# Performance work log

Measured on AMD Instinct MI355X. Metric: run time of the kernel, lower is better.

The kernel has to match this reference:

```python
import jax, jax.numpy as jnp
import numpy as np

D_MODEL = 1024
H = 16
D_K = D_MODEL // H
D_FF = 4096
EPS = 1e-6


def layer_norm(x, alpha, bias):
    mean = jnp.mean(x, axis=-1, keepdims=True)
    var = jnp.mean((x - mean) ** 2, axis=-1, keepdims=True)  # unbiased=False
    return alpha * (x - mean) / jnp.sqrt(var + EPS) + bias


def setup_inputs() -> dict:
    key = jax.random.key(0)
    ks = jax.random.split(key, 8)
    B, S = 4, 2048
    sd = 1.0 / np.sqrt(D_MODEL)
    x = jax.random.normal(ks[0], (B, S, D_MODEL), dtype=jnp.float32)
    src_mask = jnp.ones((B, 1, S), dtype=jnp.int32)
    wq = jax.random.normal(ks[1], (D_MODEL, D_MODEL), jnp.float32) * sd
    wk = jax.random.normal(ks[2], (D_MODEL, D_MODEL), jnp.float32) * sd
    wv = jax.random.normal(ks[3], (D_MODEL, D_MODEL), jnp.float32) * sd
    wo = jax.random.normal(ks[4], (D_MODEL, D_MODEL), jnp.float32) * sd
    w1 = jax.random.normal(ks[5], (D_FF, D_MODEL), jnp.float32) * sd
    b1 = jnp.zeros((D_FF,), jnp.float32)
    w2 = jax.random.normal(ks[6], (D_MODEL, D_FF), jnp.float32) * (1.0 / np.sqrt(D_FF))
    b2 = jnp.zeros((D_MODEL,), jnp.float32)
    ln1_a = jnp.ones((D_MODEL,), jnp.float32)
    ln1_b = jnp.zeros((D_MODEL,), jnp.float32)
    ln2_a = jnp.ones((D_MODEL,), jnp.float32)
    ln2_b = jnp.zeros((D_MODEL,), jnp.float32)
    return dict(x=x, src_mask=src_mask, wq=wq, wk=wk, wv=wv, wo=wo,
                ln1_a=ln1_a, ln1_b=ln1_b, ln2_a=ln2_a, ln2_b=ln2_b,
                w1=w1, b1=b1, w2=w2, b2=b2)


def attention(xn, wq, wk, wv, wo, src_mask):
    B, S, _ = xn.shape
    # torch nn.Linear: y = x @ W.T
    q = (xn @ wq.T).reshape(B, S, H, D_K).transpose(0, 2, 1, 3)  # [B,H,S,Dk]
    k = (xn @ wk.T).reshape(B, S, H, D_K).transpose(0, 2, 1, 3)
    v = (xn @ wv.T).reshape(B, S, H, D_K).transpose(0, 2, 1, 3)
    scores = jnp.einsum('bhqd,bhkd->bhqk', q, k) / np.sqrt(D_K)
    m = src_mask[:, None, :, :]  # [B,1,1,S] from [B,1,S]
    scores = jnp.where(m == 0, -jnp.inf, scores)
    attn = jax.nn.softmax(scores, axis=-1)
    out = jnp.einsum('bhqk,bhkd->bhqd', attn, v)
    out = out.transpose(0, 2, 1, 3).reshape(B, S, D_MODEL)
    return out @ wo.T


def reference(x, src_mask, wq, wk, wv, wo, ln1_a, ln1_b, ln2_a, ln2_b, w1, b1, w2, b2):
    # pre-LN residual 1: self-attention
    xn = layer_norm(x, ln1_a, ln1_b)
    x = x + attention(xn, wq, wk, wv, wo, src_mask)
    # pre-LN residual 2: FFN
    xn = layer_norm(x, ln2_a, ln2_b)
    h = jax.nn.relu(xn @ w1.T + b1)
    x = x + (h @ w2.T + b2)
    return x
```

## Files before the change

kernel.cpp:

```cpp
#include <hip/hip_runtime.h>
#include <stdint.h>

typedef unsigned short u16;
typedef __bf16 bf16x8 __attribute__((ext_vector_type(8)));
typedef float   f32x4 __attribute__((ext_vector_type(4)));
typedef u16     u16x8 __attribute__((ext_vector_type(8)));
typedef u16     u16x4 __attribute__((ext_vector_type(4)));

__device__ __forceinline__ u16 f2bf(float f) {
    union { float f; uint32_t i; } c; c.f = f;
    uint32_t r = c.i + 0x7FFFu + ((c.i >> 16) & 1u);
    return (u16)(r >> 16);
}
__device__ __forceinline__ uint32_t cvt_pk_bf16(float lo, float hi) {
    uint32_t r;
    asm("v_cvt_pk_bf16_f32 %0, %1, %2" : "=v"(r) : "v"(lo), "v"(hi));
    return r;
}
__device__ __forceinline__ void gload_lds16(const u16* g, u16* l) {
    __builtin_amdgcn_global_load_lds(
        (__attribute__((address_space(1))) void*)(g),
        (__attribute__((address_space(3))) void*)(l), 16, 0, 0);
}

__global__ __launch_bounds__(256) void cvt_all(
    const float* __restrict__ wq, const float* __restrict__ wk,
    const float* __restrict__ wv, const float* __restrict__ wo,
    const float* __restrict__ w1, const float* __restrict__ w2,
    u16* __restrict__ wqb, u16* __restrict__ wkb, u16* __restrict__ wvb,
    u16* __restrict__ wob, u16* __restrict__ w1b, u16* __restrict__ w2b)
{
    int blk = blockIdx.x;
    const float* src; u16* dst; int off;
    if      (blk < 1024)  { src = wq; dst = wqb; off = blk; }
    else if (blk < 2048)  { src = wk; dst = wkb; off = blk - 1024; }
    else if (blk < 3072)  { src = wv; dst = wvb; off = blk - 2048; }
    else if (blk < 4096)  { src = wo; dst = wob; off = blk - 3072; }
    else if (blk < 8192)  { src = w1; dst = w1b; off = blk - 4096; }
    else                  { src = w2; dst = w2b; off = blk - 8192; }
    int i = off * 1024 + threadIdx.x * 4;
    float4 v = *(const float4*)(src + i);
    u16x4 o; o[0] = f2bf(v.x); o[1] = f2bf(v.y); o[2] = f2bf(v.z); o[3] = f2bf(v.w);
    *(u16x4*)(dst + i) = o;
}

__global__ __launch_bounds__(256) void ln_kernel(
    const float* __restrict__ x, const float* __restrict__ ga,
    const float* __restrict__ be, u16* __restrict__ out)
{
    const int D = 1024;
    int row  = blockIdx.x * 4 + (threadIdx.x >> 6);
    int lane = threadIdx.x & 63;
    const float* xr = x + (size_t)row * D + lane * 16;
    float f[16];
#pragma unroll
    for (int i = 0; i < 4; ++i) *(float4*)&f[i * 4] = *(const float4*)(xr + i * 4);
    float s = 0.f, s2 = 0.f;
#pragma unroll
    for (int i = 0; i < 16; ++i) { s += f[i]; s2 += f[i] * f[i]; }
#pragma unroll
    for (int off = 1; off < 64; off <<= 1) {
        s  += __shfl_xor(s,  off, 64);
        s2 += __shfl_xor(s2, off, 64);
    }
    float mean = s * (1.0f / 1024.0f);
    float var  = s2 * (1.0f / 1024.0f) - mean * mean;
    var = var < 0.f ? 0.f : var;
    float inv = 1.0f / sqrtf(var + 1e-6f);
    float g[16], b[16];
#pragma unroll
    for (int i = 0; i < 4; ++i) {
        *(float4*)&g[i * 4] = *(const float4*)(ga + lane * 16 + i * 4);
        *(float4*)&b[i * 4] = *(const float4*)(be + lane * 16 + i * 4);
    }
    u16x8 o0, o1;
#pragma unroll
    for (int i = 0; i < 8; ++i) {
        o0[i] = f2bf(g[i]     * (f[i]     - mean) * inv + b[i]);
        o1[i] = f2bf(g[8 + i] * (f[8 + i] - mean) * inv + b[8 + i]);
    }
    u16* orow = out + (size_t)row * D + lane * 16;
    *(u16x8*)(orow)     = o0;
    *(u16x8*)(orow + 8) = o1;
}

__device__ __forceinline__ void gemm256_core(
    const u16* __restrict__ A, const u16* __restrict__ W,
    int K, int ldw, int row_a0, int row_w0,
    u16* smem, f32x4 (&acc)[4][4])
{
    int tid  = threadIdx.x;
    int lane = tid & 63;
    int quad = lane >> 4, l16 = lane & 15;
    int wave = tid >> 6;
    int wm = wave >> 2, wn = wave & 3;

    const u16* as0 = A + (size_t)(row_a0 + (tid >> 2)) * K   + (tid & 3) * 8;
    const u16* bs0 = W + (size_t)(row_w0 + (tid >> 2)) * ldw + (tid & 3) * 8;
    const u16* bs1 = bs0 + (size_t)128 * ldw;
    u16* d_a0 = smem + tid * 8;
    u16* d_a1 = smem + 4096  + tid * 8;
    u16* d_b00 = smem + 8192  + tid * 8;
    u16* d_b01 = smem + 12288 + tid * 8;
    u16* d_b10 = smem + 16384 + tid * 8;
    u16* d_b11 = smem + 20480 + tid * 8;

    const int nk = K >> 6;
    gload_lds16(as0,      d_a0);
    gload_lds16(as0 + 32, d_a1);
    gload_lds16(bs0,      d_b00);
    gload_lds16(bs0 + 32, d_b10);
    gload_lds16(bs1,      d_b01);
    gload_lds16(bs1 + 32, d_b11);
    __syncthreads();

    const int aoff = (wm * 64 + l16) * 32 + quad * 8;
    const int boff = (wn * 64 + l16) * 32 + quad * 8;

    for (int t = 0; t < nk; ++t) {
        const int cb = (t & 1) * 24576;
        if (t + 1 < nk) {
            const int nb = ((t + 1) & 1) * 24576;
            const int k0 = (t + 1) * 64;
            gload_lds16(as0 + k0,      d_a0  + nb);
            gload_lds16(as0 + k0 + 32, d_a1  + nb);
            gload_lds16(bs0 + k0,      d_b00 + nb);
            gload_lds16(bs0 + k0 + 32, d_b10 + nb);
            gload_lds16(bs1 + k0,      d_b01 + nb);
            gload_lds16(bs1 + k0 + 32, d_b11 + nb);
        }
#pragma unroll
        for (int h = 0; h < 2; ++h) {
            const u16* Ah = smem + cb + h * 4096;
            const u16* Bh = smem + cb + 8192 + h * 8192;
            bf16x8 af[4], bf[4];
#pragma unroll
            for (int mt = 0; mt < 4; ++mt)
                af[mt] = *(const bf16x8*)(&Ah[aoff + mt * 512]);
#pragma unroll
            for (int nt = 0; nt < 4; ++nt)
                bf[nt] = *(const bf16x8*)(&Bh[boff + nt * 512]);
#pragma unroll
            for (int mt = 0; mt < 4; ++mt)
#pragma unroll
                for (int nt = 0; nt < 4; ++nt)
                    acc[mt][nt] = __builtin_amdgcn_mfma_f32_16x16x32_bf16(
                        af[mt], bf[nt], acc[mt][nt], 0, 0, 0);
        }
        __syncthreads();
    }
}

template<bool OUTF32>
__global__ __launch_bounds__(512, 2) void gemm256(
    const u16* __restrict__ A, const u16* __restrict__ W,
    const float* __restrict__ bias, const float* __restrict__ resid,
    void* __restrict__ Cp, int M, int N, int K, int ldw, int do_relu)
{
    __shared__ u16 smem[49152];
    int tid  = threadIdx.x;
    int lane = tid & 63, wave = tid >> 6;
    int quad = lane >> 4, l16 = lane & 15;
    int wm = wave >> 2, wn = wave & 3;
    const int row_a0 = blockIdx.x * 128, row_w0 = blockIdx.y * 256;
    f32x4 acc[4][4] = {};
    gemm256_core(A, W, K, ldw, row_a0, row_w0, smem, acc);
#pragma unroll
    for (int mt = 0; mt < 4; ++mt) {
#pragma unroll
        for (int nt = 0; nt < 4; ++nt) {
#pragma unroll
            for (int r = 0; r < 4; ++r) {
                int grow = row_a0 + wm * 64 + mt * 16 + quad * 4 + r;
                int gcol = row_w0 + wn * 64 + nt * 16 + l16;
                float vv = acc[mt][nt][r];
                if (bias)    vv += bias[gcol];
                if (do_relu) vv = vv > 0.f ? vv : 0.f;
                if (resid)   vv += resid[(size_t)grow * N + gcol];
                if (OUTF32) ((float*)Cp)[(size_t)grow * N + gcol] = vv;
                else        ((u16*)Cp)[(size_t)grow * N + gcol] = f2bf(vv);
            }
        }
    }
}

__global__ __launch_bounds__(512, 2) void gemm256_qkv(
    const u16* __restrict__ A, const u16* __restrict__ Wqkv,
    u16* __restrict__ qo, u16* __restrict__ ko, u16* __restrict__ vo, int K)
{
    __shared__ u16 smem[49152];
    int tid  = threadIdx.x;
    int lane = tid & 63, wave = tid >> 6;
    int quad = lane >> 4, l16 = lane & 15;
    int wm = wave >> 2, wn = wave & 3;
    const int row_a0 = blockIdx.x * 128, row_w0 = blockIdx.y * 256;
    f32x4 acc[4][4] = {};
    gemm256_core(A, Wqkv, K, K, row_a0, row_w0, smem, acc);
    int seg = row_w0 >> 10;
    u16* dst = (seg == 0) ? qo : (seg == 1) ? ko : vo;
    int col0 = row_w0 & 1023;
#pragma unroll
    for (int mt = 0; mt < 4; ++mt) {
#pragma unroll
        for (int nt = 0; nt < 4; ++nt) {
#pragma unroll
            for (int r = 0; r < 4; ++r) {
                int grow = row_a0 + wm * 64 + mt * 16 + quad * 4 + r;
                int gcol = col0 + wn * 64 + nt * 16 + l16;
                dst[(size_t)grow * 1024 + gcol] = f2bf(acc[mt][nt][r]);
            }
        }
    }
}

__global__ __launch_bounds__(512, 4) void attn_kernel(
    const u16* __restrict__ Q, const u16* __restrict__ Km, const u16* __restrict__ Vm,
    const int* __restrict__ mask, u16* __restrict__ O)
{
    const int S = 2048, DM = 1024;
    const float C1 = 0.18033688f;
    const float C0 = -11.541560f;
    __shared__ u16 smem[35840];
    u16* Ks0 = smem;
    u16* Ks1 = smem + 4096;
    u16* Vt0 = smem + 8192;
    u16* Vt1 = smem + 12800;
    u16* Ps  = smem + 17408;
    u16* Qs  = smem + 17408;

    int qt = blockIdx.x, bh = blockIdx.y;
    int b = bh >> 4, h = bh & 15;
    int tid = threadIdx.x;
    int wave = tid >> 6, lane = tid & 63;
    int quad = lane >> 4, l16 = lane & 15;
    size_t base = (size_t)b * S;
    size_t hoff = (size_t)h * 64;

    {
        int r = tid >> 1, c0 = (tid & 1) * 32;
        const u16* src = Q + (base + qt * 256 + r) * DM + hoff + c0;
        u16* dq = Qs + r * 72 + c0;
        *(u16x8*)(dq)      = *(const u16x8*)(src);
        *(u16x8*)(dq + 8)  = *(const u16x8*)(src + 8);
        *(u16x8*)(dq + 16) = *(const u16x8*)(src + 16);
        *(u16x8*)(dq + 24) = *(const u16x8*)(src + 24);
    }
    const u16* ksrc = Km + (base + (tid >> 3)) * DM + hoff
                    + ((tid & 7) ^ ((tid >> 5) & 7)) * 8;
    int kp = tid & 31, d0 = (tid >> 5) * 4;
    const u16* vsrc = Vm + (base + kp * 2) * DM + hoff + d0;
    const int* msrc = mask + b * S + 4 * l16;

    __syncthreads();
    const int q0 = wave * 32;
    bf16x8 qf00 = *(const bf16x8*)(&Qs[(q0 + l16) * 72 + quad * 8]);
    bf16x8 qf01 = *(const bf16x8*)(&Qs[(q0 + l16) * 72 + 32 + quad * 8]);
    bf16x8 qf10 = *(const bf16x8*)(&Qs[(q0 + 16 + l16) * 72 + quad * 8]);
    bf16x8 qf11 = *(const bf16x8*)(&Qs[(q0 + 16 + l16) * 72 + 32 + quad * 8]);
    const int swz = (l16 & 7) * 8;
    const int u0  = (quad * 8) ^ swz;

    {
        u16x4 va = *(const u16x4*)(vsrc);
        u16x4 vb = *(const u16x4*)(vsrc + DM);
        gload_lds16(ksrc, Ks0 + tid * 8);
        ksrc += 64 * DM; vsrc += 64 * DM;
#pragma unroll
        for (int i = 0; i < 4; ++i) {
            uint32_t w = (uint32_t)va[i] | ((uint32_t)vb[i] << 16);
            *(uint32_t*)(&Vt0[(d0 + i) * 72 + kp * 2]) = w;
        }
    }
    __syncthreads();

    float l0[4] = {0.f, 0.f, 0.f, 0.f};
    float l1[4] = {0.f, 0.f, 0.f, 0.f};
    f32x4 o0[4] = {}, o1[4] = {};

    for (int it = 0; it < 32; ++it) {
        const u16* Kcur = (it & 1) ? Ks1 : Ks0;
        const u16* Vcur = (it & 1) ? Vt1 : Vt0;
        u16* Knxt = (it & 1) ? Ks0 : Ks1;
        u16* Vnxt = (it & 1) ? Vt0 : Vt1;
        const bool pfch = (it < 31);
        u16x4 va, vb;
        if (pfch) {
            va = *(const u16x4*)(vsrc);
            vb = *(const u16x4*)(vsrc + DM);
            gload_lds16(ksrc, Knxt + tid * 8);
            ksrc += 64 * DM; vsrc += 64 * DM;
        }
        f32x4 s0[4] = {}, s1[4] = {};
#pragma unroll
        for (int t = 0; t < 4; ++t) {
            const u16* krp = Kcur + (4 * l16 + t) * 64;
            bf16x8 kf0 = *(const bf16x8*)(krp + u0);
            bf16x8 kf1 = *(const bf16x8*)(krp + (u0 ^ 32));
            s0[t] = __builtin_amdgcn_mfma_f32_16x16x32_bf16(qf00, kf0, s0[t], 0, 0, 0);
            s0[t] = __builtin_amdgcn_mfma_f32_16x16x32_bf16(qf01, kf1, s0[t], 0, 0, 0);
            s1[t] = __builtin_amdgcn_mfma_f32_16x16x32_bf16(qf10, kf0, s1[t], 0, 0, 0);
            s1[t] = __builtin_amdgcn_mfma_f32_16x16x32_bf16(qf11, kf1, s1[t], 0, 0, 0);
        }
        int4 mk4 = *(const int4*)(msrc); msrc += 64;
        float c0t[4];
        c0t[0] = (mk4.x == 0) ? -1e38f : C0;
        c0t[1] = (mk4.y == 0) ? -1e38f : C0;
        c0t[2] = (mk4.z == 0) ? -1e38f : C0;
        c0t[3] = (mk4.w == 0) ? -1e38f : C0;
#pragma unroll
        for (int r = 0; r < 4; ++r) {
            float p0 = exp2f(fmaf(s0[0][r], C1, c0t[0]));
            float p1 = exp2f(fmaf(s0[1][r], C1, c0t[1]));
            float p2 = exp2f(fmaf(s0[2][r], C1, c0t[2]));
            float p3 = exp2f(fmaf(s0[3][r], C1, c0t[3]));
            l0[r] += (p0 + p1) + (p2 + p3);
            uint2 pw;
            pw.x = cvt_pk_bf16(p0, p1);
            pw.y = cvt_pk_bf16(p2, p3);
            *(uint2*)(&Ps[(q0 + quad * 4 + r) * 72 + 4 * l16]) = pw;
        }
#pragma unroll
        for (int r = 0; r < 4; ++r) {
            float p0 = exp2f(fmaf(s1[0][r], C1, c0t[0]));
            float p1 = exp2f(fmaf(s1[1][r], C1, c0t[1]));
            float p2 = exp2f(fmaf(s1[2][r], C1, c0t[2]));
            float p3 = exp2f(fmaf(s1[3][r], C1, c0t[3]));
            l1[r] += (p0 + p1) + (p2 + p3);
            uint2 pw;
            pw.x = cvt_pk_bf16(p0, p1);
            pw.y = cvt_pk_bf16(p2, p3);
            *(uint2*)(&Ps[(q0 + 16 + quad * 4 + r) * 72 + 4 * l16]) = pw;
        }
        bf16x8 pf00 = *(const bf16x8*)(&Ps[(q0 + l16) * 72 + quad * 8]);
        bf16x8 pf01 = *(const bf16x8*)(&Ps[(q0 + l16) * 72 + 32 + quad * 8]);
        bf16x8 pf10 = *(const bf16x8*)(&Ps[(q0 + 16 + l16) * 72 + quad * 8]);
        bf16x8 pf11 = *(const bf16x8*)(&Ps[(q0 + 16 + l16) * 72 + 32 + quad * 8]);
#pragma unroll
        for (int t = 0; t < 4; ++t) {
            bf16x8 vf0 = *(const bf16x8*)(&Vcur[(t * 16 + l16) * 72 + quad * 8]);
            bf16x8 vf1 = *(const bf16x8*)(&Vcur[(t * 16 + l16) * 72 + 32 + quad * 8]);
            o0[t] = __builtin_amdgcn_mfma_f32_16x16x32_bf16(pf00, vf0, o0[t], 0, 0, 0);
            o0[t] = __builtin_amdgcn_mfma_f32_16x16x32_bf16(pf01, vf1, o0[t], 0, 0, 0);
            o1[t] = __builtin_amdgcn_mfma_f32_16x16x32_bf16(pf10, vf0, o1[t], 0, 0, 0);
            o1[t] = __builtin_amdgcn_mfma_f32_16x16x32_bf16(pf11, vf1, o1[t], 0, 0, 0);
        }
        if (pfch) {
#pragma unroll
            for (int i = 0; i < 4; ++i) {
                uint32_t w = (uint32_t)va[i] | ((uint32_t)vb[i] << 16);
                *(uint32_t*)(&Vnxt[(d0 + i) * 72 + kp * 2]) = w;
            }
        }
        __syncthreads();
    }
#pragma unroll
    for (int r = 0; r < 4; ++r) {
#pragma unroll
        for (int off = 1; off < 16; off <<= 1) {
            l0[r] += __shfl_xor(l0[r], off, 16);
            l1[r] += __shfl_xor(l1[r], off, 16);
        }
        float i0 = 1.0f / l0[r];
        float i1 = 1.0f / l1[r];
        u16* dst0 = O + (base + qt * 256 + q0 + quad * 4 + r) * DM + hoff + l16;
        u16* dst1 = dst0 + (size_t)16 * DM;
#pragma unroll
        for (int t = 0; t < 4; ++t) {
            dst0[t * 16] = f2bf(o0[t][r] * i0);
            dst1[t * 16] = f2bf(o1[t][r] * i1);
        }
    }
}

extern "C" void kernel_launch(void* const* d_in, const int* in_sizes, int n_in,
                              void* d_out, int out_size, void* d_ws, size_t ws_size,
                              hipStream_t stream)
{
    (void)in_sizes; (void)n_in; (void)out_size; (void)ws_size;
    const float* x    = (const float*)d_in[0];
    const int*   mask = (const int*)d_in[1];
    const float* wq   = (const float*)d_in[2];
    const float* wk   = (const float*)d_in[3];
    const float* wv   = (const float*)d_in[4];
    const float* wo   = (const float*)d_in[5];
    const float* ln1a = (const float*)d_in[6];
    const float* ln1b = (const float*)d_in[7];
    const float* ln2a = (const float*)d_in[8];
    const float* ln2b = (const float*)d_in[9];
    const float* w1   = (const float*)d_in[10];
    const float* b1   = (const float*)d_in[11];
    const float* w2   = (const float*)d_in[12];
    const float* b2   = (const float*)d_in[13];

    const int M = 8192, D = 1024, F = 4096;
    char* ws = (char*)d_ws;
    u16*  wqkv = (u16*)(ws);
    u16*  wqb = wqkv;
    u16*  wkb = (u16*)(ws + (2u  << 20));
    u16*  wvb = (u16*)(ws + (4u  << 20));
    u16*  wob = (u16*)(ws + (6u  << 20));
    u16*  w1b = (u16*)(ws + (8u  << 20));
    u16*  w2b = (u16*)(ws + (16u << 20));
    u16*  xn  = (u16*)(ws + (24u << 20));
    u16*  q   = (u16*)(ws + (40u << 20));
    u16*  hb  = (u16*)(ws + (40u << 20));

    u16*   kbuf = (u16*)d_out;
    u16*   vbuf = (u16*)d_out + (size_t)M * D;
    float* x1   = (float*)d_out;

    cvt_all<<<12288, 256, 0, stream>>>(wq, wk, wv, wo, w1, w2,
                                       wqb, wkb, wvb, wob, w1b, w2b);

    ln_kernel<<<M / 4, 256, 0, stream>>>(x, ln1a, ln1b, xn);
    dim3 gq(M / 128, 3072 / 256);
    gemm256_qkv<<<gq, 512, 0, stream>>>(xn, wqkv, q, kbuf, vbuf, D);
    dim3 ga(2048 / 256, 64);
    attn_kernel<<<ga, 512, 0, stream>>>(q, kbuf, vbuf, mask, xn);
    dim3 g1(M / 128, D / 256);
    gemm256<true ><<<g1, 512, 0, stream>>>(xn, wob, nullptr, x, x1, M, D, D, D, 0);
    ln_kernel<<<M / 4, 256, 0, stream>>>(x1, ln2a, ln2b, xn);
    dim3 gf1(M / 128, 2048 / 256);
    dim3 gf2(M / 128, D / 256);
    gemm256<false><<<gf1, 512, 0, stream>>>(xn, w1b, b1, nullptr, hb, M, 2048, D, D, 1);
    gemm256<true ><<<gf2, 512, 0, stream>>>(hb, w2b, nullptr, x1, x1, M, D, 2048, F, 0);
    gemm256<false><<<gf1, 512, 0, stream>>>(xn, w1b + (size_t)2048 * D, b1 + 2048, nullptr, hb, M, 2048, D, D, 1);
    gemm256<true ><<<gf2, 512, 0, stream>>>(hb, w2b + 2048, b2, x1, x1, M, D, 2048, F, 0);
}
```

Baseline: 587.3 us.

## Shrink GEMM tiles to 128x128 with triple-buffered K=32 LDS pipeline

```diff
diff --git a/kernel.cpp b/kernel.cpp
--- a/kernel.cpp
+++ b/kernel.cpp
@@ -21,6 +21,10 @@
     __builtin_amdgcn_global_load_lds(
         (__attribute__((address_space(1))) void*)(g),
         (__attribute__((address_space(3))) void*)(l), 16, 0, 0);
+}
+template<int N>
+__device__ __forceinline__ void wait_vm_barrier() {
+    asm volatile("s_waitcnt vmcnt(%0)\n\ts_barrier" :: "n"(N) : "memory");
 }
 
 __global__ __launch_bounds__(256) void cvt_all(
@@ -84,10 +88,10 @@
     *(u16x8*)(orow + 8) = o1;
 }
 
-__device__ __forceinline__ void gemm256_core(
+__device__ __forceinline__ void gemm128q_core(
     const u16* __restrict__ A, const u16* __restrict__ W,
     int K, int ldw, int row_a0, int row_w0,
-    u16* smem, f32x4 (&acc)[4][4])
+    u16* smem, f32x4 (&acc)[4][2])
 {
     int tid  = threadIdx.x;
     int lane = tid & 63;
@@ -95,84 +99,69 @@
     int wave = tid >> 6;
     int wm = wave >> 2, wn = wave & 3;
 
-    const u16* as0 = A + (size_t)(row_a0 + (tid >> 2)) * K   + (tid & 3) * 8;
-    const u16* bs0 = W + (size_t)(row_w0 + (tid >> 2)) * ldw + (tid & 3) * 8;
-    const u16* bs1 = bs0 + (size_t)128 * ldw;
-    u16* d_a0 = smem + tid * 8;
-    u16* d_a1 = smem + 4096  + tid * 8;
-    u16* d_b00 = smem + 8192  + tid * 8;
-    u16* d_b01 = smem + 12288 + tid * 8;
-    u16* d_b10 = smem + 16384 + tid * 8;
-    u16* d_b11 = smem + 20480 + tid * 8;
-
-    const int nk = K >> 6;
-    gload_lds16(as0,      d_a0);
-    gload_lds16(as0 + 32, d_a1);
-    gload_lds16(bs0,      d_b00);
-    gload_lds16(bs0 + 32, d_b10);
-    gload_lds16(bs1,      d_b01);
-    gload_lds16(bs1 + 32, d_b11);
-    __syncthreads();
-
-    const int aoff = (wm * 64 + l16) * 32 + quad * 8;
-    const int boff = (wn * 64 + l16) * 32 + quad * 8;
-
+    const u16* a0 = A + (size_t)(row_a0 + (tid >> 2)) * K   + (tid & 3) * 8;
+    const u16* b0 = W + (size_t)(row_w0 + (tid >> 2)) * ldw + (tid & 3) * 8;
+    u16* dst = smem + tid * 8;
+    const int nk = K >> 5;
+
+#pragma unroll
+    for (int s = 0; s < 3; ++s) {
+        gload_lds16(a0 + s * 32, dst + s * 8192);
+        gload_lds16(b0 + s * 32, dst + s * 8192 + 4096);
+    }
+    const int abase = (wm * 64 + l16) * 32 + quad * 8;
+    const int bbase = 4096 + (wn * 32 + l16) * 32 + quad * 8;
+    wait_vm_barrier<4>();
+
+    int cb = 0, nb = 16384;
     for (int t = 0; t < nk; ++t) {
-        const int cb = (t & 1) * 24576;
-        if (t + 1 < nk) {
-            const int nb = ((t + 1) & 1) * 24576;
-            const int k0 = (t + 1) * 64;
-            gload_lds16(as0 + k0,      d_a0  + nb);
-            gload_lds16(as0 + k0 + 32, d_a1  + nb);
-            gload_lds16(bs0 + k0,      d_b00 + nb);
-            gload_lds16(bs0 + k0 + 32, d_b10 + nb);
-            gload_lds16(bs1 + k0,      d_b01 + nb);
-            gload_lds16(bs1 + k0 + 32, d_b11 + nb);
-        }
-#pragma unroll
-        for (int h = 0; h < 2; ++h) {
-            const u16* Ah = smem + cb + h * 4096;
-            const u16* Bh = smem + cb + 8192 + h * 8192;
-            bf16x8 af[4], bf[4];
-#pragma unroll
-            for (int mt = 0; mt < 4; ++mt)
-                af[mt] = *(const bf16x8*)(&Ah[aoff + mt * 512]);
-#pragma unroll
-            for (int nt = 0; nt < 4; ++nt)
-                bf[nt] = *(const bf16x8*)(&Bh[boff + nt * 512]);
-#pragma unroll
-            for (int mt = 0; mt < 4; ++mt)
-#pragma unroll
-                for (int nt = 0; nt < 4; ++nt)
-                    acc[mt][nt] = __builtin_amdgcn_mfma_f32_16x16x32_bf16(
-                        af[mt], bf[nt], acc[mt][nt], 0, 0, 0);
-        }
-        __syncthreads();
+        if (t + 2 < nk) {
+            gload_lds16(a0 + (t + 2) * 32, dst + nb);
+            gload_lds16(b0 + (t + 2) * 32, dst + nb + 4096);
+        }
+        const u16* buf = smem + cb;
+        bf16x8 af[4], bf[2];
+#pragma unroll
+        for (int mt = 0; mt < 4; ++mt)
+            af[mt] = *(const bf16x8*)(&buf[abase + mt * 512]);
+#pragma unroll
+        for (int nt = 0; nt < 2; ++nt)
+            bf[nt] = *(const bf16x8*)(&buf[bbase + nt * 512]);
+#pragma unroll
+        for (int mt = 0; mt < 4; ++mt)
+#pragma unroll
+            for (int nt = 0; nt < 2; ++nt)
+                acc[mt][nt] = __builtin_amdgcn_mfma_f32_16x16x32_bf16(
+                    af[mt], bf[nt], acc[mt][nt], 0, 0, 0);
+        if      (t + 2 < nk) wait_vm_barrier<2>();
+        else if (t + 1 < nk) wait_vm_barrier<0>();
+        cb = (cb == 16384) ? 0 : cb + 8192;
+        nb = (nb == 16384) ? 0 : nb + 8192;
     }
 }
 
 template<bool OUTF32>
-__global__ __launch_bounds__(512, 2) void gemm256(
+__global__ __launch_bounds__(512, 4) void gemm128q(
     const u16* __restrict__ A, const u16* __restrict__ W,
     const float* __restrict__ bias, const float* __restrict__ resid,
     void* __restrict__ Cp, int M, int N, int K, int ldw, int do_relu)
 {
-    __shared__ u16 smem[49152];
+    __shared__ u16 smem[24576];
     int tid  = threadIdx.x;
     int lane = tid & 63, wave = tid >> 6;
     int quad = lane >> 4, l16 = lane & 15;
     int wm = wave >> 2, wn = wave & 3;
-    const int row_a0 = blockIdx.x * 128, row_w0 = blockIdx.y * 256;
-    f32x4 acc[4][4] = {};
-    gemm256_core(A, W, K, ldw, row_a0, row_w0, smem, acc);
+    const int row_a0 = blockIdx.x * 128, row_w0 = blockIdx.y * 128;
+    f32x4 acc[4][2] = {};
+    gemm128q_core(A, W, K, ldw, row_a0, row_w0, smem, acc);
 #pragma unroll
     for (int mt = 0; mt < 4; ++mt) {
 #pragma unroll
-        for (int nt = 0; nt < 4; ++nt) {
+        for (int nt = 0; nt < 2; ++nt) {
 #pragma unroll
             for (int r = 0; r < 4; ++r) {
                 int grow = row_a0 + wm * 64 + mt * 16 + quad * 4 + r;
-                int gcol = row_w0 + wn * 64 + nt * 16 + l16;
+                int gcol = row_w0 + wn * 32 + nt * 16 + l16;
                 float vv = acc[mt][nt][r];
                 if (bias)    vv += bias[gcol];
                 if (do_relu) vv = vv > 0.f ? vv : 0.f;
@@ -184,29 +173,29 @@
     }
 }
 
-__global__ __launch_bounds__(512, 2) void gemm256_qkv(
+__global__ __launch_bounds__(512, 4) void gemm128q_qkv(
     const u16* __restrict__ A, const u16* __restrict__ Wqkv,
     u16* __restrict__ qo, u16* __restrict__ ko, u16* __restrict__ vo, int K)
 {
-    __shared__ u16 smem[49152];
+    __shared__ u16 smem[24576];
     int tid  = threadIdx.x;
     int lane = tid & 63, wave = tid >> 6;
     int quad = lane >> 4, l16 = lane & 15;
     int wm = wave >> 2, wn = wave & 3;
-    const int row_a0 = blockIdx.x * 128, row_w0 = blockIdx.y * 256;
-    f32x4 acc[4][4] = {};
-    gemm256_core(A, Wqkv, K, K, row_a0, row_w0, smem, acc);
+    const int row_a0 = blockIdx.x * 128, row_w0 = blockIdx.y * 128;
+    f32x4 acc[4][2] = {};
+    gemm128q_core(A, Wqkv, K, K, row_a0, row_w0, smem, acc);
     int seg = row_w0 >> 10;
     u16* dst = (seg == 0) ? qo : (seg == 1) ? ko : vo;
     int col0 = row_w0 & 1023;
 #pragma unroll
     for (int mt = 0; mt < 4; ++mt) {
 #pragma unroll
-        for (int nt = 0; nt < 4; ++nt) {
+        for (int nt = 0; nt < 2; ++nt) {
 #pragma unroll
             for (int r = 0; r < 4; ++r) {
                 int grow = row_a0 + wm * 64 + mt * 16 + quad * 4 + r;
-                int gcol = col0 + wn * 64 + nt * 16 + l16;
+                int gcol = col0 + wn * 32 + nt * 16 + l16;
                 dst[(size_t)grow * 1024 + gcol] = f2bf(acc[mt][nt][r]);
             }
         }
@@ -413,17 +402,17 @@
                                        wqb, wkb, wvb, wob, w1b, w2b);
 
     ln_kernel<<<M / 4, 256, 0, stream>>>(x, ln1a, ln1b, xn);
-    dim3 gq(M / 128, 3072 / 256);
-    gemm256_qkv<<<gq, 512, 0, stream>>>(xn, wqkv, q, kbuf, vbuf, D);
+    dim3 gq(M / 128, 3072 / 128);
+    gemm128q_qkv<<<gq, 512, 0, stream>>>(xn, wqkv, q, kbuf, vbuf, D);
     dim3 ga(2048 / 256, 64);
     attn_kernel<<<ga, 512, 0, stream>>>(q, kbuf, vbuf, mask, xn);
-    dim3 g1(M / 128, D / 256);
-    gemm256<true ><<<g1, 512, 0, stream>>>(xn, wob, nullptr, x, x1, M, D, D, D, 0);
+    dim3 g1(M / 128, D / 128);
+    gemm128q<true ><<<g1, 512, 0, stream>>>(xn, wob, nullptr, x, x1, M, D, D, D, 0);
     ln_kernel<<<M / 4, 256, 0, stream>>>(x1, ln2a, ln2b, xn);
-    dim3 gf1(M / 128, 2048 / 256);
-    dim3 gf2(M / 128, D / 256);
-    gemm256<false><<<gf1, 512, 0, stream>>>(xn, w1b, b1, nullptr, hb, M, 2048, D, D, 1);
-    gemm256<true ><<<gf2, 512, 0, stream>>>(hb, w2b, nullptr, x1, x1, M, D, 2048, F, 0);
-    gemm256<false><<<gf1, 512, 0, stream>>>(xn, w1b + (size_t)2048 * D, b1 + 2048, nullptr, hb, M, 2048, D, D, 1);
-    gemm256<true ><<<gf2, 512, 0, stream>>>(hb, w2b + 2048, b2, x1, x1, M, D, 2048, F, 0);
-}
+    dim3 gf1(M / 128, 2048 / 128);
+    dim3 gf2(M / 128, D / 128);
+    gemm128q<false><<<gf1, 512, 0, stream>>>(xn, w1b, b1, nullptr, hb, M, 2048, D, D, 1);
+    gemm128q<true ><<<gf2, 512, 0, stream>>>(hb, w2b, nullptr, x1, x1, M, D, 2048, F, 0);
+    gemm128q<false><<<gf1, 512, 0, stream>>>(xn, w1b + (size_t)2048 * D, b1 + 2048, nullptr, hb, M, 2048, D, D, 1);
+    gemm128q<true ><<<gf2, 512, 0, stream>>>(hb, w2b + 2048, b2, x1, x1, M, D, 2048, F, 0);
+}
```

Result: faster. 561.8 us (-4.3%).
